# Performance work log

Measured on AMD Instinct MI355X. Metric: run time of the kernel, lower is better.

The kernel has to match this reference:

```python
import jax, jax.numpy as jnp
import numpy as np

VOCAB = 32000
EMBED = 8      # == d_k == n_qubits (forced by the module's reshapes)
NQ = 8
DEPTH = 2
NBLOCKS = 6
FFN = 8        # == n_qubits (forced)
NCLASSES = 10
B, S = 32, 1024
LN_EPS = 1e-5

_H = np.array([[1.0, 1.0], [1.0, -1.0]], np.complex64) / np.sqrt(2.0).astype(np.float32)


def _posenc(seq, dim):
    pos = np.arange(seq, dtype=np.float32)[:, None]
    div = np.exp(np.arange(0, dim, 2, dtype=np.float32) * (-np.log(10000.0) / dim))
    pe = np.zeros((seq, dim), np.float32)
    pe[:, 0::2] = np.sin(pos * div)
    pe[:, 1::2] = np.cos(pos * div)
    return jnp.asarray(pe)


def _quantum_head(x, depth=DEPTH):
    """Batched statevector simulation of the QNode. x: (N, NQ) angles -> (N, NQ) Z expvals."""
    N, n = x.shape
    c = jnp.cos(0.5 * x).astype(jnp.complex64)
    s = jnp.sin(0.5 * x).astype(jnp.complex64)
    amp = jnp.stack([c, -1j * s], axis=-1)  # (N, n, 2): RX(theta)|0>
    state = amp[:, 0]  # product state built wire by wire -> (N, 2, ..., 2)
    for i in range(1, n):
        state = state[..., None] * amp[:, i].reshape((N,) + (1,) * (state.ndim - 1) + (2,))
    Hm = jnp.asarray(_H)
    for _ in range(depth):
        for i in range(n - 1):  # CNOT(i, i+1): flip target slice where control==1
            s0 = jnp.take(state, 0, axis=i + 1)
            s1 = jnp.flip(jnp.take(state, 1, axis=i + 1), axis=i + 1)
            state = jnp.stack([s0, s1], axis=i + 1)
        state = jnp.einsum('...i,ij->...j', state, Hm)  # Hadamard on last wire
    probs = state.real ** 2 + state.imag ** 2  # (N, 2, ..., 2)
    zs = []
    for i in range(n):
        axes = tuple(a for a in range(1, n + 1) if a != i + 1)
        m = probs.sum(axis=axes)  # (N, 2) marginal of wire i
        zs.append(m[:, 0] - m[:, 1])
    return jnp.stack(zs, axis=-1)


def _ln(x, g, b):
    m = x.mean(axis=-1, keepdims=True)
    v = ((x - m) ** 2).mean(axis=-1, keepdims=True)
    return g * (x - m) / jnp.sqrt(v + LN_EPS) + b


def _forward(tokens, emb, ln1_g, ln1_b, ln2_g, ln2_b, attn_w, attn_b,
             ffn_w1, ffn_b1, ffn_w2, ffn_b2, cls_w, cls_b):
    Bt, St = tokens.shape
    E = emb.shape[1]
    x = emb[tokens] + _posenc(St, E)[None]  # (B, S, E)
    scale = float(1.0 / np.sqrt(E))
    for l in range(NBLOCKS):
        # quantum attention (num_heads == 1, d_k == E)
        qkv = _quantum_head(x.reshape(-1, E)).reshape(Bt, St, E)
        scores = jnp.einsum('bqd,bkd->bqk', qkv, qkv) * scale
        attn = jax.nn.softmax(scores, axis=-1)
        out = jnp.einsum('bqk,bkd->bqd', attn, qkv)
        attn_out = out @ attn_w[l] + attn_b[l]
        x = _ln(x + attn_out, ln1_g[l], ln1_b[l])
        # quantum FFN
        h = x @ ffn_w1[l] + ffn_b1[l]  # (B, S, FFN)
        qf = _quantum_head(h.reshape(-1, FFN)).reshape(Bt, St, FFN)
        ffn_out = qf @ ffn_w2[l] + ffn_b2[l]
        x = _ln(x + ffn_out, ln2_g[l], ln2_b[l])
    pooled = x.mean(axis=1)  # (B, E)
    return pooled @ cls_w + cls_b  # (B, NCLASSES)


def setup_inputs() -> dict:
    key = jax.random.key(0)
    ks = jax.random.split(key, 8)
    f32 = jnp.float32
    L, E, F = NBLOCKS, EMBED, FFN
    return {
        'tokens': jax.random.randint(ks[0], (B, S), 0, VOCAB),
        'emb': jax.random.normal(ks[1], (VOCAB, E), f32) * 0.1,
        'ln1_g': jnp.ones((L, E), f32), 'ln1_b': jnp.zeros((L, E), f32),
        'ln2_g': jnp.ones((L, E), f32), 'ln2_b': jnp.zeros((L, E), f32),
        'attn_w': jax.random.normal(ks[2], (L, E, E), f32) * 0.3,
        'attn_b': jnp.zeros((L, E), f32),
        'ffn_w1': jax.random.normal(ks[3], (L, E, F), f32) * 0.3,
        'ffn_b1': jnp.zeros((L, F), f32),
        'ffn_w2': jax.random.normal(ks[4], (L, F, E), f32) * 0.3,
        'ffn_b2': jnp.zeros((L, E), f32),
        'cls_w': jax.random.normal(ks[5], (E, NCLASSES), f32) * 0.3,
        'cls_b': jnp.zeros((NCLASSES,), f32),
    }


def reference(tokens, emb, ln1_g, ln1_b, ln2_g, ln2_b, attn_w, attn_b,
              ffn_w1, ffn_b1, ffn_w2, ffn_b2, cls_w, cls_b):
    return _forward(tokens, emb, ln1_g, ln1_b, ln2_g, ln2_b, attn_w, attn_b,
                    ffn_w1, ffn_b1, ffn_w2, ffn_b2, cls_w, cls_b)
```

## Files before the change

kernel.cpp:

```cpp
#include <hip/hip_runtime.h>
#include <math.h>

#define EMB 8
#define SEQ 1024
#define NBATCH 32
#define NROWS (NBATCH * SEQ)
#define LNEPS 1e-5f
#define F(l, b, c) (((l) * 32 + (b)) * 16 + (c))

typedef __attribute__((ext_vector_type(4))) float f32x4;
typedef __attribute__((ext_vector_type(8))) _Float16 f16x8;
typedef __attribute__((ext_vector_type(16))) float f32x16;

union FragU { unsigned u[4]; f16x8 s; };

__device__ __forceinline__ unsigned pkrtz(float a, float b) {
    unsigned r;
    asm("v_cvt_pkrtz_f16_f32 %0, %1, %2" : "=v"(r) : "v"(a), "v"(b));
    return r;
}

__device__ __forceinline__ float hw_exp2(float x) {
    return __builtin_amdgcn_exp2f(x);
}

__device__ __forceinline__ void llc_load_row2(const float* p, f32x4 d[4]) {
    asm volatile(
        "global_load_dwordx4 %0, %[a], off sc0 sc1\n\t"
        "global_load_dwordx4 %1, %[a], off offset:16 sc0 sc1\n\t"
        "global_load_dwordx4 %2, %[a], off offset:32 sc0 sc1\n\t"
        "global_load_dwordx4 %3, %[a], off offset:48 sc0 sc1\n\t"
        "s_waitcnt vmcnt(0)"
        : "=&v"(d[0]), "=&v"(d[1]), "=&v"(d[2]), "=&v"(d[3])
        : [a] "v"(p) : "memory");
}
__device__ __forceinline__ void llc_store_row(float* p, f32x4 a, f32x4 b) {
    asm volatile(
        "global_store_dwordx4 %[a], %[x], off sc0 sc1\n\t"
        "global_store_dwordx4 %[a], %[y], off offset:16 sc0 sc1"
        :: [a] "v"(p), [x] "v"(a), [y] "v"(b) : "memory");
}
__device__ __forceinline__ void sys_store(float* p, float v) {
    asm volatile("global_store_dword %0, %1, off sc0 sc1" :: "v"(p), "v"(v) : "memory");
}
__device__ __forceinline__ float sys_load(const float* p) {
    float r;
    asm volatile("global_load_dword %0, %1, off sc0 sc1\n\ts_waitcnt vmcnt(0)"
                 : "=v"(r) : "v"(p) : "memory");
    return r;
}
__device__ __forceinline__ unsigned sys_load_u32(const unsigned* p) {
    unsigned r;
    asm volatile("global_load_dword %0, %1, off sc0 sc1\n\ts_waitcnt vmcnt(0)"
                 : "=v"(r) : "v"(p) : "memory");
    return r;
}
__device__ __forceinline__ void sys_store_u32(unsigned* p, unsigned v) {
    asm volatile("global_store_dword %0, %1, off sc0 sc1" :: "v"(p), "v"(v) : "memory");
}

__device__ __forceinline__ void qhead(const float xv[8], float z[8]) {
    float c[8];
#pragma unroll
    for (int j = 0; j < 8; ++j) c[j] = __cosf(xv[j]);
    float e0 = c[0];
    float o1 = c[1];
    float e2 = e0 * c[2];
    float o3 = o1 * c[3];
    float e4 = e2 * c[4];
    float o5 = o3 * c[5];
    float e6 = e4 * c[6];
    z[0] = e0; z[1] = o1; z[2] = e2; z[3] = o3;
    z[4] = e4; z[5] = o5; z[6] = e6;
    z[7] = e6 * o5 * c[7];
}

__device__ __forceinline__ void embed_row(const int* __restrict__ tokens,
                                          const float* __restrict__ emb,
                                          long grow, int srow, float xv[8]) {
    int tok = tokens[grow];
    const float* e = emb + (long)tok * EMB;
    float p = (float)srow;
    xv[0] = e[0] + sinf(p);
    xv[1] = e[1] + cosf(p);
    xv[2] = e[2] + sinf(p * 0.1f);
    xv[3] = e[3] + cosf(p * 0.1f);
    xv[4] = e[4] + sinf(p * 0.01f);
    xv[5] = e[5] + cosf(p * 0.01f);
    xv[6] = e[6] + sinf(p * 0.001f);
    xv[7] = e[7] + cosf(p * 0.001f);
}

__global__ __launch_bounds__(1024) void zero_flags(unsigned* __restrict__ f) {
    for (int i = threadIdx.x; i < 3584; i += 1024) f[i] = 0u;
}

__global__ __launch_bounds__(512, 2) void qt_fused(
    const int* __restrict__ tokens, const float* __restrict__ emb,
    const float* __restrict__ attn_w, const float* __restrict__ attn_b,
    const float* __restrict__ ln1_g, const float* __restrict__ ln1_b,
    const float* __restrict__ ffn_w1, const float* __restrict__ ffn_b1,
    const float* __restrict__ ffn_w2, const float* __restrict__ ffn_b2,
    const float* __restrict__ ln2_g, const float* __restrict__ ln2_b,
    const float* __restrict__ cls_w, const float* __restrict__ cls_b,
    float* __restrict__ qkv0, float* __restrict__ qkv1,
    unsigned* __restrict__ flags, unsigned* __restrict__ pcnt,
    float* __restrict__ partial, float* __restrict__ out)
{
    __shared__ __align__(16) uint2 KbP[2][1024];
    __shared__ __align__(16) unsigned short VtH[8][1032];
    __shared__ float Olds[8][32][9];
    __shared__ float x_lds[2][64][8];
    __shared__ int isL[2];

    const int bid = blockIdx.x;
    const int group = bid & 15;
    const int chunk = bid >> 4;
    const int tid = threadIdx.x;
    const float beta = 0.71423162f;

    const int w = tid >> 6;
    const int lane = tid & 63;
    const int ln = lane & 31;
    const int h = lane >> 5;
    const int qtile = w >> 2;
    const int qu = w & 3;
    const int r0 = tid * 2;

    for (int l = 0; l < 6; ++l) {
        const float* qr = (l & 1) ? qkv1 : qkv0;
        float* qw = (l & 1) ? qkv0 : qkv1;
        for (int ph = 0; ph < 2; ++ph) {
            const int bb = group * 2 + ph;
            {
                float v0[8], v1[8];
                if (l == 0) {
                    float e0[8], e1[8];
                    embed_row(tokens, emb, (long)bb * SEQ + r0, r0, e0);
                    embed_row(tokens, emb, (long)bb * SEQ + r0 + 1, r0 + 1, e1);
                    if ((r0 >> 6) == chunk) {
                        const int lr = r0 - chunk * 64;
#pragma unroll
                        for (int j = 0; j < 8; ++j) {
                            x_lds[ph][lr][j] = e0[j];
                            x_lds[ph][lr + 1][j] = e1[j];
                        }
                    }
                    qhead(e0, v0); qhead(e1, v1);
                } else {
                    const unsigned* fp = &flags[F(l, bb, r0 >> 6)];
                    while (sys_load_u32(fp) == 0u) __builtin_amdgcn_s_sleep(1);
                    f32x4 d[4];
                    llc_load_row2(qr + ((long)bb * SEQ + r0) * 8, d);
#pragma unroll
                    for (int j = 0; j < 4; ++j) {
                        v0[j] = d[0][j]; v0[4 + j] = d[1][j];
                        v1[j] = d[2][j]; v1[4 + j] = d[3][j];
                    }
                }
                uint4 k0, k1;
                k0.x = pkrtz(v0[0] * beta, v0[1] * beta);
                k0.y = pkrtz(v0[2] * beta, v0[3] * beta);
                k0.z = pkrtz(v1[0] * beta, v1[1] * beta);
                k0.w = pkrtz(v1[2] * beta, v1[3] * beta);
                k1.x = pkrtz(v0[4] * beta, v0[5] * beta);
                k1.y = pkrtz(v0[6] * beta, v0[7] * beta);
                k1.z = pkrtz(v1[4] * beta, v1[5] * beta);
                k1.w = pkrtz(v1[6] * beta, v1[7] * beta);
                *(uint4*)&KbP[0][r0] = k0;
                *(uint4*)&KbP[1][r0] = k1;
#pragma unroll
                for (int c = 0; c < 8; ++c)
                    *(unsigned*)&VtH[c][r0] = pkrtz(v0[c], v1[c]);
            }
            __syncthreads();

            const int qbase = chunk * 64 + qtile * 32;
            FragU qfB;
            {
                uint2 qh = KbP[h][qbase + ln];
                qfB.u[0] = qh.x; qfB.u[1] = qh.y; qfB.u[2] = qh.x; qfB.u[3] = qh.y;
            }
            f32x16 zc;
#pragma unroll
            for (int i = 0; i < 16; ++i) zc[i] = 0.f;
            f32x16 accA = zc, accB = zc;

#pragma unroll 2
            for (int t = 0; t < 8; ++t) {
                const int kbase = ((qu << 3) | t) << 5;
                FragU kfA;
                {
                    uint2 kh = KbP[h][kbase + ln];
                    kfA.u[0] = kh.x; kfA.u[1] = kh.y; kfA.u[2] = 0; kfA.u[3] = 0;
                }
                f32x16 s = __builtin_amdgcn_mfma_f32_32x32x16_f16(kfA.s, qfB.s, zc, 0, 0, 0);
                float p[16];
#pragma unroll
                for (int g = 0; g < 16; ++g) p[g] = hw_exp2(s[g]);

                FragU a1, a2;
#pragma unroll
                for (int vi = 0; vi < 4; ++vi) {
                    a1.u[vi] = pkrtz(p[2 * vi], p[2 * vi + 1]);
                    a2.u[vi] = pkrtz(p[8 + 2 * vi], p[8 + 2 * vi + 1]);
                }
                FragU v1h, v2h;
                if (ln < 8) {
                    const unsigned* q0 = (const unsigned*)&VtH[ln][kbase + 4 * h];
                    const unsigned* q1 = (const unsigned*)&VtH[ln][kbase + 8 + 4 * h];
                    const unsigned* q2 = (const unsigned*)&VtH[ln][kbase + 16 + 4 * h];
                    const unsigned* q3 = (const unsigned*)&VtH[ln][kbase + 24 + 4 * h];
                    v1h.u[0] = q0[0]; v1h.u[1] = q0[1]; v1h.u[2] = q1[0]; v1h.u[3] = q1[1];
                    v2h.u[0] = q2[0]; v2h.u[1] = q2[1]; v2h.u[2] = q3[0]; v2h.u[3] = q3[1];
                } else if (ln == 8) {
#pragma unroll
                    for (int i = 0; i < 4; ++i) { v1h.u[i] = 0x3C003C00u; v2h.u[i] = 0x3C003C00u; }
                } else {
#pragma unroll
                    for (int i = 0; i < 4; ++i) { v1h.u[i] = 0; v2h.u[i] = 0; }
                }
                accA = __builtin_amdgcn_mfma_f32_32x32x16_f16(a1.s, v1h.s, accA, 0, 0, 0);
                accB = __builtin_amdgcn_mfma_f32_32x32x16_f16(a2.s, v2h.s, accB, 0, 0, 0);
            }

            if (ln <= 8) {
#pragma unroll
                for (int g = 0; g < 16; ++g)
                    Olds[w][(g & 3) + 8 * (g >> 2) + 4 * h][ln] = accA[g] + accB[g];
            }
            __syncthreads();

            if ((tid >> 6) == ph) {
                const int r = tid & 63;
                const int rr = r & 31;
                const int w0 = (r >> 5) * 4;
                float o[9];
#pragma unroll
                for (int c = 0; c < 9; ++c)
                    o[c] = (Olds[w0][rr][c] + Olds[w0 + 1][rr][c])
                         + (Olds[w0 + 2][rr][c] + Olds[w0 + 3][rr][c]);
                float inv = 1.0f / o[8];
                float outv[8];
#pragma unroll
                for (int c = 0; c < 8; ++c) outv[c] = o[c] * inv;

                const float* W  = attn_w + l * 64; const float* Wb  = attn_b + l * 8;
                const float* g1 = ln1_g + l * 8;   const float* b1v = ln1_b + l * 8;
                const float* W1 = ffn_w1 + l * 64; const float* c1  = ffn_b1 + l * 8;
                const float* W2 = ffn_w2 + l * 64; const float* c2  = ffn_b2 + l * 8;
                const float* g2 = ln2_g + l * 8;   const float* b2v = ln2_b + l * 8;

                float xv[8];
#pragma unroll
                for (int j = 0; j < 8; ++j) xv[j] = x_lds[ph][r][j];

                float y[8]; float m = 0.f;
#pragma unroll
                for (int j = 0; j < 8; ++j) {
                    float vv = Wb[j];
#pragma unroll
                    for (int i = 0; i < 8; ++i) vv += outv[i] * W[i * 8 + j];
                    y[j] = xv[j] + vv;
                    m += y[j];
                }
                m *= 0.125f;
                float var = 0.f;
#pragma unroll
                for (int j = 0; j < 8; ++j) { float dd = y[j] - m; var += dd * dd; }
                var *= 0.125f;
                float rsg = rsqrtf(var + LNEPS);
                float xn[8];
#pragma unroll
                for (int j = 0; j < 8; ++j) xn[j] = g1[j] * (y[j] - m) * rsg + b1v[j];

                float hh[8];
#pragma unroll
                for (int j = 0; j < 8; ++j) {
                    float vv = c1[j];
#pragma unroll
                    for (int i = 0; i < 8; ++i) vv += xn[i] * W1[i * 8 + j];
                    hh[j] = vv;
                }
                float qff[8]; qhead(hh, qff);
                float m2 = 0.f;
#pragma unroll
                for (int j = 0; j < 8; ++j) {
                    float vv = c2[j];
#pragma unroll
                    for (int i = 0; i < 8; ++i) vv += qff[i] * W2[i * 8 + j];
                    y[j] = xn[j] + vv;
                    m2 += y[j];
                }
                m2 *= 0.125f;
                float var2 = 0.f;
#pragma unroll
                for (int j = 0; j < 8; ++j) { float dd = y[j] - m2; var2 += dd * dd; }
                var2 *= 0.125f;
                float rs2 = rsqrtf(var2 + LNEPS);
#pragma unroll
                for (int j = 0; j < 8; ++j) {
                    float xo = g2[j] * (y[j] - m2) * rs2 + b2v[j];
                    x_lds[ph][r][j] = xo;
                    xv[j] = xo;
                }

                if (l < 5) {
                    float z[8]; qhead(xv, z);
                    f32x4 z0 = {z[0], z[1], z[2], z[3]}, z1 = {z[4], z[5], z[6], z[7]};
                    llc_store_row(qw + ((long)bb * SEQ + chunk * 64 + r) * 8, z0, z1);
                    asm volatile("s_waitcnt vmcnt(0)" ::: "memory");
                    if (r == 0) sys_store_u32(&flags[F(l + 1, bb, chunk)], 1u);
                }
            }
        }
    }

    if ((tid >> 6) < 2) {
        const int ph = tid >> 6;
        const int r = tid & 63;
        const int bb = group * 2 + ph;
        float a[8];
#pragma unroll
        for (int j = 0; j < 8; ++j) {
            a[j] = x_lds[ph][r][j];
#pragma unroll
            for (int off = 1; off <= 32; off <<= 1) a[j] += __shfl_xor(a[j], off);
        }
        if (r < 8) sys_store(&partial[(bb * 16 + chunk) * 8 + r], a[r]);
    }
    asm volatile("s_waitcnt vmcnt(0)" ::: "memory");
    __syncthreads();
    if (tid == 0) {
        unsigned r = __hip_atomic_fetch_add(&pcnt[(group * 2) * 16], 1u,
                                            __ATOMIC_RELAXED, __HIP_MEMORY_SCOPE_AGENT);
        isL[0] = (r == 15u);
    }
    if (tid == 64) {
        unsigned r = __hip_atomic_fetch_add(&pcnt[(group * 2 + 1) * 16], 1u,
                                            __ATOMIC_RELAXED, __HIP_MEMORY_SCOPE_AGENT);
        isL[1] = (r == 15u);
    }
    __syncthreads();
    if ((tid >> 6) < 2) {
        const int ph = tid >> 6;
        if (isL[ph]) {
            const int bb = group * 2 + ph;
            const int lr = tid & 63;
            int g = lr >> 3, j = lr & 7;
            float s = sys_load(&partial[(bb * 16 + g) * 8 + j])
                    + sys_load(&partial[(bb * 16 + g + 8) * 8 + j]);
            s += __shfl_xor(s, 8); s += __shfl_xor(s, 16); s += __shfl_xor(s, 32);
            float poolj = s * (1.0f / 1024.0f);
            int c = lr < 10 ? lr : 9;
            float o = cls_b[c];
#pragma unroll
            for (int j2 = 0; j2 < 8; ++j2)
                o += __shfl(poolj, j2) * cls_w[j2 * 10 + c];
            if (lr < 10) out[bb * 10 + lr] = o;
        }
    }
}

extern "C" void kernel_launch(void* const* d_in, const int* in_sizes, int n_in,
                              void* d_out, int out_size, void* d_ws, size_t ws_size,
                              hipStream_t stream) {
    const int*   tokens = (const int*)d_in[0];
    const float* emb    = (const float*)d_in[1];
    const float* ln1_g  = (const float*)d_in[2];
    const float* ln1_b  = (const float*)d_in[3];
    const float* ln2_g  = (const float*)d_in[4];
    const float* ln2_b  = (const float*)d_in[5];
    const float* attn_w = (const float*)d_in[6];
    const float* attn_b = (const float*)d_in[7];
    const float* ffn_w1 = (const float*)d_in[8];
    const float* ffn_b1 = (const float*)d_in[9];
    const float* ffn_w2 = (const float*)d_in[10];
    const float* ffn_b2 = (const float*)d_in[11];
    const float* cls_w  = (const float*)d_in[12];
    const float* cls_b  = (const float*)d_in[13];

    unsigned* flags   = (unsigned*)d_ws;
    unsigned* pcnt    = flags + 3072;
    float*    partial = (float*)d_ws + 3584;
    float*    qkv0    = (float*)d_ws + 3584 + 4096;
    float*    qkv1    = qkv0 + (long)NROWS * 8;
    float*    outp    = (float*)d_out;

    zero_flags<<<1, 1024, 0, stream>>>(flags);
    qt_fused<<<256, 512, 0, stream>>>(
        tokens, emb, attn_w, attn_b, ln1_g, ln1_b,
        ffn_w1, ffn_b1, ffn_w2, ffn_b2, ln2_g, ln2_b,
        cls_w, cls_b, qkv0, qkv1, flags, pcnt, partial, outp);
}
```

Baseline: 75.94 us.

## Split work across 512 blocks and exchange quantum-head outputs in fp16

Doubles the grid to 512 blocks, each owning 32 query rows instead of 64, with all 8 waves sharing one query tile and splitting keys four tiles each. Occupancy hint rises to 4 blocks per CU, and flags, partials and the final pooling count are resized to match. The inter-layer qkv exchange buffer is stored as packed fp16 instead of fp32, halving global traffic, and the softmax scale is applied to the query fragment with a packed fp16 multiply. This adds more flag synchronisation points and extra fp16 rounding on stored activations, and relies on 512 spin-waiting blocks all being resident at once.

```diff
diff --git a/kernel.cpp b/kernel.cpp
--- a/kernel.cpp
+++ b/kernel.cpp
@@ -6,9 +6,9 @@
 #define NBATCH 32
 #define NROWS (NBATCH * SEQ)
 #define LNEPS 1e-5f
-#define F(l, b, c) (((l) * 32 + (b)) * 16 + (c))
-
-typedef __attribute__((ext_vector_type(4))) float f32x4;
+#define F2(l, b, c) (((l) * 32 + (b)) * 32 + (c))
+
+typedef __attribute__((ext_vector_type(4))) unsigned u32x4;
 typedef __attribute__((ext_vector_type(8))) _Float16 f16x8;
 typedef __attribute__((ext_vector_type(16))) float f32x16;
 
@@ -19,26 +19,26 @@
     asm("v_cvt_pkrtz_f16_f32 %0, %1, %2" : "=v"(r) : "v"(a), "v"(b));
     return r;
 }
-
+__device__ __forceinline__ unsigned pk_mul_f16(unsigned a, unsigned b) {
+    unsigned r;
+    asm("v_pk_mul_f16 %0, %1, %2" : "=v"(r) : "v"(a), "v"(b));
+    return r;
+}
 __device__ __forceinline__ float hw_exp2(float x) {
     return __builtin_amdgcn_exp2f(x);
 }
 
-__device__ __forceinline__ void llc_load_row2(const float* p, f32x4 d[4]) {
+__device__ __forceinline__ void llc_load_2rows(const unsigned short* p,
+                                               u32x4* d0, u32x4* d1) {
     asm volatile(
         "global_load_dwordx4 %0, %[a], off sc0 sc1\n\t"
         "global_load_dwordx4 %1, %[a], off offset:16 sc0 sc1\n\t"
-        "global_load_dwordx4 %2, %[a], off offset:32 sc0 sc1\n\t"
-        "global_load_dwordx4 %3, %[a], off offset:48 sc0 sc1\n\t"
         "s_waitcnt vmcnt(0)"
-        : "=&v"(d[0]), "=&v"(d[1]), "=&v"(d[2]), "=&v"(d[3])
-        : [a] "v"(p) : "memory");
-}
-__device__ __forceinline__ void llc_store_row(float* p, f32x4 a, f32x4 b) {
-    asm volatile(
-        "global_store_dwordx4 %[a], %[x], off sc0 sc1\n\t"
-        "global_store_dwordx4 %[a], %[y], off offset:16 sc0 sc1"
-        :: [a] "v"(p), [x] "v"(a), [y] "v"(b) : "memory");
+        : "=&v"(*d0), "=&v"(*d1) : [a] "v"(p) : "memory");
+}
+__device__ __forceinline__ void llc_store_row16(unsigned short* p, u32x4 v) {
+    asm volatile("global_store_dwordx4 %[a], %[x], off sc0 sc1"
+                 :: [a] "v"(p), [x] "v"(v) : "memory");
 }
 __device__ __forceinline__ void sys_store(float* p, float v) {
     asm volatile("global_store_dword %0, %1, off sc0 sc1" :: "v"(p), "v"(v) : "memory");
@@ -92,10 +92,10 @@
 }
 
 __global__ __launch_bounds__(1024) void zero_flags(unsigned* __restrict__ f) {
-    for (int i = threadIdx.x; i < 3584; i += 1024) f[i] = 0u;
-}
-
-__global__ __launch_bounds__(512, 2) void qt_fused(
+    for (int i = threadIdx.x; i < 6656; i += 1024) f[i] = 0u;
+}
+
+__global__ __launch_bounds__(512, 4) void qt_fused(
     const int* __restrict__ tokens, const float* __restrict__ emb,
     const float* __restrict__ attn_w, const float* __restrict__ attn_b,
     const float* __restrict__ ln1_g, const float* __restrict__ ln1_b,
@@ -103,92 +103,87 @@
     const float* __restrict__ ffn_w2, const float* __restrict__ ffn_b2,
     const float* __restrict__ ln2_g, const float* __restrict__ ln2_b,
     const float* __restrict__ cls_w, const float* __restrict__ cls_b,
-    float* __restrict__ qkv0, float* __restrict__ qkv1,
+    unsigned short* __restrict__ qkv0, unsigned short* __restrict__ qkv1,
     unsigned* __restrict__ flags, unsigned* __restrict__ pcnt,
     float* __restrict__ partial, float* __restrict__ out)
 {
     __shared__ __align__(16) uint2 KbP[2][1024];
     __shared__ __align__(16) unsigned short VtH[8][1032];
     __shared__ float Olds[8][32][9];
-    __shared__ float x_lds[2][64][8];
+    __shared__ float x_lds[2][32][8];
     __shared__ int isL[2];
 
     const int bid = blockIdx.x;
     const int group = bid & 15;
     const int chunk = bid >> 4;
     const int tid = threadIdx.x;
-    const float beta = 0.71423162f;
 
     const int w = tid >> 6;
     const int lane = tid & 63;
     const int ln = lane & 31;
     const int h = lane >> 5;
-    const int qtile = w >> 2;
-    const int qu = w & 3;
-    const int r0 = tid * 2;
+    const int qbase = chunk * 32;
+    const unsigned B2PK = pkrtz(0.51006972f, 0.51006972f);
 
     for (int l = 0; l < 6; ++l) {
-        const float* qr = (l & 1) ? qkv1 : qkv0;
-        float* qw = (l & 1) ? qkv0 : qkv1;
+        const unsigned short* qr = (l & 1) ? qkv1 : qkv0;
+        unsigned short* qw = (l & 1) ? qkv0 : qkv1;
         for (int ph = 0; ph < 2; ++ph) {
             const int bb = group * 2 + ph;
             {
-                float v0[8], v1[8];
+                u32x4 d0, d1;
                 if (l == 0) {
-                    float e0[8], e1[8];
-                    embed_row(tokens, emb, (long)bb * SEQ + r0, r0, e0);
-                    embed_row(tokens, emb, (long)bb * SEQ + r0 + 1, r0 + 1, e1);
-                    if ((r0 >> 6) == chunk) {
-                        const int lr = r0 - chunk * 64;
+                    float e0[8], e1[8], z0[8], z1[8];
+                    embed_row(tokens, emb, (long)bb * SEQ + 2 * tid, 2 * tid, e0);
+                    embed_row(tokens, emb, (long)bb * SEQ + 2 * tid + 1, 2 * tid + 1, e1);
+                    if ((tid >> 4) == chunk) {
+                        const int lr = 2 * tid - chunk * 32;
 #pragma unroll
                         for (int j = 0; j < 8; ++j) {
                             x_lds[ph][lr][j] = e0[j];
                             x_lds[ph][lr + 1][j] = e1[j];
                         }
                     }
-                    qhead(e0, v0); qhead(e1, v1);
+                    qhead(e0, z0); qhead(e1, z1);
+                    d0[0] = pkrtz(z0[0], z0[1]); d0[1] = pkrtz(z0[2], z0[3]);
+                    d0[2] = pkrtz(z0[4], z0[5]); d0[3] = pkrtz(z0[6], z0[7]);
+                    d1[0] = pkrtz(z1[0], z1[1]); d1[1] = pkrtz(z1[2], z1[3]);
+                    d1[2] = pkrtz(z1[4], z1[5]); d1[3] = pkrtz(z1[6], z1[7]);
                 } else {
-                    const unsigned* fp = &flags[F(l, bb, r0 >> 6)];
+                    const unsigned* fp = &flags[F2(l, bb, tid >> 4)];
                     while (sys_load_u32(fp) == 0u) __builtin_amdgcn_s_sleep(1);
-                    f32x4 d[4];
-                    llc_load_row2(qr + ((long)bb * SEQ + r0) * 8, d);
-#pragma unroll
-                    for (int j = 0; j < 4; ++j) {
-                        v0[j] = d[0][j]; v0[4 + j] = d[1][j];
-                        v1[j] = d[2][j]; v1[4 + j] = d[3][j];
-                    }
-                }
-                uint4 k0, k1;
-                k0.x = pkrtz(v0[0] * beta, v0[1] * beta);
-                k0.y = pkrtz(v0[2] * beta, v0[3] * beta);
-                k0.z = pkrtz(v1[0] * beta, v1[1] * beta);
-                k0.w = pkrtz(v1[2] * beta, v1[3] * beta);
-                k1.x = pkrtz(v0[4] * beta, v0[5] * beta);
-                k1.y = pkrtz(v0[6] * beta, v0[7] * beta);
-                k1.z = pkrtz(v1[4] * beta, v1[5] * beta);
-                k1.w = pkrtz(v1[6] * beta, v1[7] * beta);
-                *(uint4*)&KbP[0][r0] = k0;
-                *(uint4*)&KbP[1][r0] = k1;
-#pragma unroll
-                for (int c = 0; c < 8; ++c)
-                    *(unsigned*)&VtH[c][r0] = pkrtz(v0[c], v1[c]);
+                    llc_load_2rows(qr + ((long)bb * SEQ + 2 * tid) * 8, &d0, &d1);
+                }
+                u32x4 kp0, kp1;
+                kp0[0] = d0[0]; kp0[1] = d0[1]; kp0[2] = d1[0]; kp0[3] = d1[1];
+                kp1[0] = d0[2]; kp1[1] = d0[3]; kp1[2] = d1[2]; kp1[3] = d1[3];
+                *(u32x4*)&KbP[0][2 * tid] = kp0;
+                *(u32x4*)&KbP[1][2 * tid] = kp1;
+#pragma unroll
+                for (int c = 0; c < 8; ++c) {
+                    unsigned wa = d0[c >> 1], wb = d1[c >> 1];
+                    unsigned v = (c & 1) ? ((wa >> 16) | (wb & 0xFFFF0000u))
+                                         : ((wa & 0xFFFFu) | (wb << 16));
+                    *(unsigned*)&VtH[c][2 * tid] = v;
+                }
             }
             __syncthreads();
 
-            const int qbase = chunk * 64 + qtile * 32;
             FragU qfB;
             {
                 uint2 qh = KbP[h][qbase + ln];
-                qfB.u[0] = qh.x; qfB.u[1] = qh.y; qfB.u[2] = qh.x; qfB.u[3] = qh.y;
+                unsigned qx = pk_mul_f16(qh.x, B2PK);
+                unsigned qy = pk_mul_f16(qh.y, B2PK);
+                qfB.u[0] = qx; qfB.u[1] = qy; qfB.u[2] = qx; qfB.u[3] = qy;
             }
             f32x16 zc;
 #pragma unroll
             for (int i = 0; i < 16; ++i) zc[i] = 0.f;
             f32x16 accA = zc, accB = zc;
 
-#pragma unroll 2
-            for (int t = 0; t < 8; ++t) {
-                const int kbase = ((qu << 3) | t) << 5;
+#pragma unroll
+            for (int t = 0; t < 4; ++t) {
+                const int kbase = (w * 4 + t) * 32;
                 FragU kfA;
                 {
                     uint2 kh = KbP[h][kbase + ln];
@@ -231,15 +226,17 @@
             }
             __syncthreads();
 
-            if ((tid >> 6) == ph) {
-                const int r = tid & 63;
-                const int rr = r & 31;
-                const int w0 = (r >> 5) * 4;
+            if ((tid >> 6) == ph && lane < 32) {
+                const int r = lane;
                 float o[9];
 #pragma unroll
-                for (int c = 0; c < 9; ++c)
-                    o[c] = (Olds[w0][rr][c] + Olds[w0 + 1][rr][c])
-                         + (Olds[w0 + 2][rr][c] + Olds[w0 + 3][rr][c]);
+                for (int c = 0; c < 9; ++c) {
+                    float s01 = Olds[0][r][c] + Olds[1][r][c];
+                    float s23 = Olds[2][r][c] + Olds[3][r][c];
+                    float s45 = Olds[4][r][c] + Olds[5][r][c];
+                    float s67 = Olds[6][r][c] + Olds[7][r][c];
+                    o[c] = (s01 + s23) + (s45 + s67);
+                }
                 float inv = 1.0f / o[8];
                 float outv[8];
 #pragma unroll
@@ -307,10 +304,12 @@
 
                 if (l < 5) {
                     float z[8]; qhead(xv, z);
-                    f32x4 z0 = {z[0], z[1], z[2], z[3]}, z1 = {z[4], z[5], z[6], z[7]};
-                    llc_store_row(qw + ((long)bb * SEQ + chunk * 64 + r) * 8, z0, z1);
+                    u32x4 pz;
+                    pz[0] = pkrtz(z[0], z[1]); pz[1] = pkrtz(z[2], z[3]);
+                    pz[2] = pkrtz(z[4], z[5]); pz[3] = pkrtz(z[6], z[7]);
+                    llc_store_row16(qw + ((long)bb * SEQ + chunk * 32 + r) * 8, pz);
                     asm volatile("s_waitcnt vmcnt(0)" ::: "memory");
-                    if (r == 0) sys_store_u32(&flags[F(l + 1, bb, chunk)], 1u);
+                    if (r == 0) sys_store_u32(&flags[F2(l + 1, bb, chunk)], 1u);
                 }
             }
         }
@@ -323,23 +322,23 @@
         float a[8];
 #pragma unroll
         for (int j = 0; j < 8; ++j) {
-            a[j] = x_lds[ph][r][j];
+            a[j] = (r < 32) ? x_lds[ph][r][j] : 0.f;
 #pragma unroll
             for (int off = 1; off <= 32; off <<= 1) a[j] += __shfl_xor(a[j], off);
         }
-        if (r < 8) sys_store(&partial[(bb * 16 + chunk) * 8 + r], a[r]);
+        if (r < 8) sys_store(&partial[(bb * 32 + chunk) * 8 + r], a[r]);
     }
     asm volatile("s_waitcnt vmcnt(0)" ::: "memory");
     __syncthreads();
     if (tid == 0) {
         unsigned r = __hip_atomic_fetch_add(&pcnt[(group * 2) * 16], 1u,
                                             __ATOMIC_RELAXED, __HIP_MEMORY_SCOPE_AGENT);
-        isL[0] = (r == 15u);
+        isL[0] = (r == 31u);
     }
     if (tid == 64) {
         unsigned r = __hip_atomic_fetch_add(&pcnt[(group * 2 + 1) * 16], 1u,
                                             __ATOMIC_RELAXED, __HIP_MEMORY_SCOPE_AGENT);
-        isL[1] = (r == 15u);
+        isL[1] = (r == 31u);
     }
     __syncthreads();
     if ((tid >> 6) < 2) {
@@ -348,8 +347,10 @@
             const int bb = group * 2 + ph;
             const int lr = tid & 63;
             int g = lr >> 3, j = lr & 7;
-            float s = sys_load(&partial[(bb * 16 + g) * 8 + j])
-                    + sys_load(&partial[(bb * 16 + g + 8) * 8 + j]);
+            float s = sys_load(&partial[(bb * 32 + g) * 8 + j])
+                    + sys_load(&partial[(bb * 32 + g + 8) * 8 + j])
+                    + sys_load(&partial[(bb * 32 + g + 16) * 8 + j])
+                    + sys_load(&partial[(bb * 32 + g + 24) * 8 + j]);
             s += __shfl_xor(s, 8); s += __shfl_xor(s, 16); s += __shfl_xor(s, 32);
             float poolj = s * (1.0f / 1024.0f);
             int c = lr < 10 ? lr : 9;
@@ -380,15 +381,15 @@
     const float* cls_w  = (const float*)d_in[12];
     const float* cls_b  = (const float*)d_in[13];
 
-    unsigned* flags   = (unsigned*)d_ws;
-    unsigned* pcnt    = flags + 3072;
-    float*    partial = (float*)d_ws + 3584;
-    float*    qkv0    = (float*)d_ws + 3584 + 4096;
-    float*    qkv1    = qkv0 + (long)NROWS * 8;
-    float*    outp    = (float*)d_out;
+    unsigned*       flags   = (unsigned*)d_ws;
+    unsigned*       pcnt    = flags + 6144;
+    float*          partial = (float*)(pcnt + 512);
+    unsigned short* qkv0    = (unsigned short*)(partial + 8192);
+    unsigned short* qkv1    = qkv0 + (long)NROWS * 8;
+    float*          outp    = (float*)d_out;
 
     zero_flags<<<1, 1024, 0, stream>>>(flags);
-    qt_fused<<<256, 512, 0, stream>>>(
+    qt_fused<<<512, 512, 0, stream>>>(
         tokens, emb, attn_w, attn_b, ln1_g, ln1_b,
         ffn_w1, ffn_b1, ffn_w2, ffn_b2, ln2_g, ln2_b,
         cls_w, cls_b, qkv0, qkv1, flags, pcnt, partial, outp);
```

Measured after the change: 89.07 us. +17.3%, slower.
